# Optimization experiments

Hardware: AMD Instinct MI355X
Metric: run time of the kernel (lower is better)

Reference implementation:

```python
import jax, jax.numpy as jnp
import numpy as np

N = 8192      # nodes
E = 262144    # edges (avg degree 32)
D = 128       # embed dim
F = 128       # input feature dim
H = 128       # GCN hidden
C = 7         # classes
EPS = 1e-4    # sample_bias for concrete noise


def setup_inputs() -> dict:
    key = jax.random.key(0)
    ks = jax.random.split(key, 10)
    x = jax.random.normal(ks[0], (N, F), jnp.float32)
    embed = jax.random.normal(ks[1], (N, D), jnp.float32)
    row = jax.random.randint(ks[2], (E,), 0, N, jnp.int64)
    col = jax.random.randint(ks[3], (E,), 0, N, jnp.int64)
    adj_data = jnp.ones((E,), jnp.float32)
    # uniform noise in (bias, 1-bias) as in concrete_sample(training=True)
    noise = jax.random.uniform(ks[4], (E,), jnp.float32, EPS, 1.0 - EPS)
    tmp = jnp.ones((1,), jnp.float32)  # temperature beta
    W1e = jax.random.normal(ks[5], (3 * D, 64), jnp.float32) * 0.05
    b1e = jnp.zeros((64,), jnp.float32)
    W2e = jax.random.normal(ks[6], (64, 1), jnp.float32) * 0.05
    b2e = jnp.zeros((1,), jnp.float32)
    Wg0 = jax.random.normal(ks[7], (F, H), jnp.float32) * 0.05
    Wg1 = jax.random.normal(ks[8], (H, C), jnp.float32) * 0.05
    return {"x": x, "embed": embed, "adj_data": adj_data, "noise": noise,
            "tmp": tmp, "W1e": W1e, "b1e": b1e, "W2e": W2e, "b2e": b2e,
            "Wg0": Wg0, "Wg1": Wg1, "row": row, "col": col, "nodeid": 5}


def reference(x, embed, adj_data, noise, tmp, W1e, b1e, W2e, b2e, Wg0, Wg1,
              row, col, nodeid):
    # gather node embeddings per edge + self node embedding, concat -> [E, 3D]
    f1 = embed[row]
    f2 = embed[col]
    selfemb = jnp.broadcast_to(embed[nodeid][None, :], (f1.shape[0], D))
    f12self = jnp.concatenate([f1, f2, selfemb], axis=-1)
    # 2-layer explainer MLP -> per-edge logit
    h = jax.nn.relu(f12self @ W1e + b1e)
    log_alpha = (h @ W2e + b2e).reshape(-1)  # [E]
    # concrete-sigmoid reparameterization (training=True path, noise supplied)
    gate_inputs = (jnp.log(noise) - jnp.log1p(-noise) + log_alpha) / tmp[0]
    values = jax.nn.sigmoid(gate_inputs)
    # scatter edge gates and adjacency values into dense [N, N]
    mask = jnp.zeros((N, N), jnp.float32).at[row, col].add(values)
    adj = jnp.zeros((N, N), jnp.float32).at[row, col].add(adj_data)
    # symmetrize mask, apply to adjacency, zero the diagonal
    sym_mask = (mask + mask.T) * 0.5
    masked_adj = adj * sym_mask * (1.0 - jnp.eye(N, dtype=jnp.float32))
    # wrapped GNN: 2-layer GCN
    h1 = jax.nn.relu(masked_adj @ (x @ Wg0))
    out = masked_adj @ (h1 @ Wg1)
    node_pred = out[nodeid]  # [C]
    return jax.nn.softmax(node_pred, axis=0)
```

## Files before the change

### kernel.cpp

```cpp
#include <hip/hip_runtime.h>
#include <hip/hip_bf16.h>
#include <math.h>

#define NNODES 8192
#define DIM 128
#define SMAX 128
#define HSIZE 16384
#define NBD 256
#define NTD 1024
#define LDA 132

__device__ __forceinline__ int detect64(const void* rowp) {
    const long long* p = (const long long*)rowp;
    int is64 = 1;
#pragma unroll
    for (int i = 0; i < 4; i++) {
        long long v = p[i];
        if (v < 0 || v >= NNODES) is64 = 0;
    }
    return is64;
}

__device__ __forceinline__ int edge_idx(const void* p, int e, int idx64) {
    if (idx64) return (int)((const long long*)p)[e];
    return ((const int*)p)[e];
}

__device__ __forceinline__ int hash_insert(unsigned int* hashK, unsigned int key1) {
    unsigned int h = (key1 * 2654435761u) & (HSIZE - 1);
    for (;;) {
        unsigned int prev = atomicCAS(&hashK[h], 0u, key1);
        if (prev == 0u || prev == key1) return (int)h;
        h = (h + 1) & (HSIZE - 1);
    }
}

__global__ __launch_bounds__(256) void k_zero(float4* z, int n4) {
    int i = blockIdx.x * blockDim.x + threadIdx.x;
    if (i < n4) z[i] = make_float4(0.f, 0.f, 0.f, 0.f);
}

__global__ __launch_bounds__(NTD) void k_dense(
        const float* embed, const float* x, const float* W1e, const float* b1e,
        const float* Wg0, const int* nodep, const void* rowp, const void* colp,
        const float* adjd,
        float* U, float* V, float* xw, float* cself,
        int* flags, float* cnt0, int* nbr, int* slotmap, int E) {
    int bid = blockIdx.x;
    int t = threadIdx.x;
    int w = t >> 6;
    int lane = t & 63;
    int nodeid = nodep[0];
    __shared__ float smf[64 * LDA];
    __shared__ float semb[DIM];

    int tile = bid;
    const float* src = (tile < 128) ? embed + (size_t)tile * 64 * DIM
                                    : x + (size_t)(tile - 128) * 64 * DIM;
    for (int i = t; i < 64 * DIM; i += NTD)
        smf[(i >> 7) * LDA + (i & 127)] = src[i];
    if (bid == 255 && t < DIM) semb[t] = embed[(size_t)nodeid * DIM + t];
    __syncthreads();

    const float* Wsrc;
    float* outp;
    int ldw, ldo, cb, doff;
    if (tile < 128) {
        Wsrc = W1e; ldw = 64; ldo = 64;
        if (w < 8) { doff = 0;   cb = w * 8;       outp = U; }
        else       { doff = 128; cb = (w - 8) * 8; outp = V; }
    } else {
        Wsrc = Wg0; ldw = DIM; ldo = DIM; doff = 0; cb = w * 8; outp = xw;
    }

    int row = lane;
    float acc[8] = {0, 0, 0, 0, 0, 0, 0, 0};
    for (int d0 = 0; d0 < DIM; d0 += 8) {
        float wb = Wsrc[(size_t)(doff + d0 + (lane >> 3)) * ldw + cb + (lane & 7)];
        float4 a0 = *(const float4*)&smf[row * LDA + d0];
        float4 a1 = *(const float4*)&smf[row * LDA + d0 + 4];
#pragma unroll
        for (int k = 0; k < 8; k++) {
            float a = (k < 4) ? (&a0.x)[k] : (&a1.x)[k - 4];
#pragma unroll
            for (int j = 0; j < 8; j++) {
                float wv = __uint_as_float(
                    __builtin_amdgcn_readlane(__float_as_uint(wb), k * 8 + j));
                acc[j] = fmaf(a, wv, acc[j]);
            }
        }
    }
    int n0 = (tile < 128 ? tile : tile - 128) * 64;
    float* orow = outp + (size_t)(n0 + row) * ldo + cb;
    *(float4*)orow       = make_float4(acc[0], acc[1], acc[2], acc[3]);
    *(float4*)(orow + 4) = make_float4(acc[4], acc[5], acc[6], acc[7]);

    if (bid == 255 && t < 64) {
        float a = b1e[t];
        for (int d = 0; d < DIM; d++)
            a += semb[d] * W1e[(size_t)(2 * DIM + d) * 64 + t];
        cself[t] = a;
    }
    int idx64 = detect64(rowp);
    int e = bid * NTD + t;
    if (e < E) {
        int r = edge_idx(rowp, e, idx64);
        if (r == nodeid) {
            int c = edge_idx(colp, e, idx64);
            if (c != nodeid) {
                atomicAdd(&cnt0[c], adjd[e]);
                if (atomicCAS((unsigned int*)&slotmap[c], 0u, 0xFFFFFFFFu) == 0u) {
                    int s = atomicAdd(&flags[1], 1);
                    if (s < SMAX) {
                        nbr[s] = c;
                        __hip_atomic_store(&slotmap[c], s + 1, __ATOMIC_RELAXED,
                                           __HIP_MEMORY_SCOPE_AGENT);
                    }
                }
            }
        }
    }
}

__global__ __launch_bounds__(1024) void k_gates(
        const float* adjd, const float* noise, const float* tmp,
        const float* W2e, const float* b2e,
        const void* rowp, const void* colp, const int* nodep,
        const float* U, const float* V, const float* cself,
        const int* slotmap,
        unsigned int* hashK, float* hashC, float* hashF, float* hashR,
        float* f0s, float* r0s, int E) {
    int idx64 = detect64(rowp);
    int nodeid = nodep[0];
    int e = blockIdx.x * blockDim.x + threadIdx.x;
    if (e >= E) return;
    int r = edge_idx(rowp, e, idx64);
    int c = edge_idx(colp, e, idx64);
    if (r == c) return;
    int spr = slotmap[r];
    int spc = slotmap[c];
    bool fr = spr > 0, fc = spc > 0;
    if (!fr && !fc) return;
    float la = b2e[0];
    const float4* u4 = (const float4*)(U + (size_t)r * 64);
    const float4* v4 = (const float4*)(V + (size_t)c * 64);
    const float4* c4 = (const float4*)cself;
    const float4* w4 = (const float4*)W2e;
#pragma unroll
    for (int d = 0; d < 16; d++) {
        float4 uu = u4[d], vv = v4[d], cc = c4[d], ww = w4[d];
        float h0 = uu.x + vv.x + cc.x;
        float h1 = uu.y + vv.y + cc.y;
        float h2 = uu.z + vv.z + cc.z;
        float h3 = uu.w + vv.w + cc.w;
        la += (h0 > 0.f ? h0 : 0.f) * ww.x + (h1 > 0.f ? h1 : 0.f) * ww.y
            + (h2 > 0.f ? h2 : 0.f) * ww.z + (h3 > 0.f ? h3 : 0.f) * ww.w;
    }
    float nz = noise[e];
    float gi = (logf(nz) - log1pf(-nz) + la) / tmp[0];
    float v = 1.f / (1.f + expf(-gi));
    if (fr) {
        int sr = spr - 1;
        unsigned int key1 = ((unsigned int)(sr << 13) | (unsigned int)c) + 1u;
        int idx = hash_insert(hashK, key1);
        atomicAdd(&hashC[idx], adjd[e]);
        atomicAdd(&hashF[idx], v);
        if (c == nodeid) atomicAdd(&r0s[sr], v);
    }
    if (fc) {
        int sc = spc - 1;
        unsigned int key1 = ((unsigned int)(sc << 13) | (unsigned int)r) + 1u;
        int idx = hash_insert(hashK, key1);
        atomicAdd(&hashR[idx], v);
        if (r == nodeid) atomicAdd(&f0s[sc], v);
    }
}

__global__ __launch_bounds__(1024) void k_hagg(
        const unsigned int* hashK, const float* hashC, const float* hashF,
        const float* hashR, const float* xw, float* h1acc) {
    int gid = blockIdx.x * blockDim.x + threadIdx.x;
    int group = gid >> 7;
    int tg = gid & 127;
    int ngroups = (256 * 1024) >> 7;
    for (int entry = group; entry < HSIZE; entry += ngroups) {
        unsigned int key1 = hashK[entry];
        if (key1 == 0u) continue;
        float wgt = hashC[entry] * (hashF[entry] + hashR[entry]) * 0.5f;
        if (wgt == 0.f) continue;
        unsigned int key = key1 - 1u;
        int s = (int)(key >> 13);
        int k = (int)(key & 8191u);
        atomicAdd(&h1acc[(size_t)s * DIM + tg], wgt * xw[(size_t)k * DIM + tg]);
    }
}

__global__ __launch_bounds__(1024) void k_final(
        const int* flags, const float* h1acc, const float* cnt0, const int* nbr,
        const float* f0s, const float* r0s, const float* Wg1, float* out) {
    int t = threadIdx.x;
    __shared__ float sacc[7];
    if (t < 7) sacc[t] = 0.f;
    __syncthreads();
    int ns = flags[1]; if (ns > SMAX) ns = SMAX;
    int wave = t >> 6, lane = t & 63;
    for (int s = wave; s < ns; s += 16) {
        float a0 = cnt0[nbr[s]] * (f0s[s] + r0s[s]) * 0.5f;
        float v0 = h1acc[(size_t)s * DIM + lane];
        float v1 = h1acc[(size_t)s * DIM + lane + 64];
        v0 = v0 > 0.f ? v0 : 0.f;
        v1 = v1 > 0.f ? v1 : 0.f;
        float part[7];
        for (int c = 0; c < 7; c++) {
            float p = v0 * Wg1[lane * 7 + c] + v1 * Wg1[(lane + 64) * 7 + c];
            for (int o = 32; o >= 1; o >>= 1) p += __shfl_xor(p, o, 64);
            part[c] = p;
        }
        if (lane == 0)
            for (int c = 0; c < 7; c++) atomicAdd(&sacc[c], a0 * part[c]);
    }
    __syncthreads();
    if (t == 0) {
        float v[7], m = -1e30f, ssum = 0.f;
        for (int c = 0; c < 7; c++) { v[c] = sacc[c]; if (v[c] > m) m = v[c]; }
        for (int c = 0; c < 7; c++) { v[c] = expf(v[c] - m); ssum += v[c]; }
        for (int c = 0; c < 7; c++) out[c] = v[c] / ssum;
    }
}

extern "C" void kernel_launch(void* const* d_in, const int* in_sizes, int n_in,
                              void* d_out, int out_size, void* d_ws, size_t ws_size,
                              hipStream_t stream) {
    const float* x     = (const float*)d_in[0];
    const float* embed = (const float*)d_in[1];
    const float* adjd  = (const float*)d_in[2];
    const float* noise = (const float*)d_in[3];
    const float* tmp   = (const float*)d_in[4];
    const float* W1e   = (const float*)d_in[5];
    const float* b1e   = (const float*)d_in[6];
    const float* W2e   = (const float*)d_in[7];
    const float* b2e   = (const float*)d_in[8];
    const float* Wg0   = (const float*)d_in[9];
    const float* Wg1   = (const float*)d_in[10];
    const void*  rowp  = d_in[11];
    const void*  colp  = d_in[12];
    const int*   nodep = (const int*)d_in[13];
    int E = in_sizes[3];

    char* w = (char*)d_ws;
    size_t off = 0;
    auto alloc = [&](size_t bytes) -> char* {
        char* p = w + off;
        off = (off + bytes + 255) & ~(size_t)255;
        return p;
    };
    float*        cself   = (float*)alloc(64 * 4);
    int*          nbr     = (int*)  alloc(SMAX * 4);
    float*        U       = (float*)alloc((size_t)NNODES * 64 * 4);
    float*        V       = (float*)alloc((size_t)NNODES * 64 * 4);
    float*        xw      = (float*)alloc((size_t)NNODES * DIM * 4);
    char*         zstart  = w + off;
    int*          flags   = (int*)  alloc(256);
    int*          slotmap = (int*)  alloc((size_t)NNODES * 4);
    float*        cnt0    = (float*)alloc((size_t)NNODES * 4);
    float*        f0s     = (float*)alloc(SMAX * 4);
    float*        r0s     = (float*)alloc(SMAX * 4);
    unsigned int* hashK   = (unsigned int*)alloc((size_t)HSIZE * 4);
    float*        hashC   = (float*)alloc((size_t)HSIZE * 4);
    float*        hashF   = (float*)alloc((size_t)HSIZE * 4);
    float*        hashR   = (float*)alloc((size_t)HSIZE * 4);
    float*        h1acc   = (float*)alloc((size_t)SMAX * DIM * 4);
    size_t zbytes  = (size_t)((w + off) - zstart);
    int n4 = (int)(zbytes / 16);

    k_zero<<<(n4 + 255) / 256, 256, 0, stream>>>((float4*)zstart, n4);
    k_dense<<<NBD, NTD, 0, stream>>>(embed, x, W1e, b1e, Wg0, nodep, rowp, colp,
                                     adjd, U, V, xw, cself, flags, cnt0, nbr,
                                     slotmap, E);
    k_gates<<<E / 1024, 1024, 0, stream>>>(adjd, noise, tmp, W2e, b2e,
                                           rowp, colp, nodep, U, V, cself,
                                           slotmap, hashK, hashC, hashF, hashR,
                                           f0s, r0s, E);
    k_hagg<<<256, 1024, 0, stream>>>(hashK, hashC, hashF, hashR, xw, h1acc);
    k_final<<<1, 1024, 0, stream>>>(flags, h1acc, cnt0, nbr, f0s, r0s, Wg1,
                                    (float*)d_out);
}
```

Before: 53.38 us.

## Retile dense GEMM with LDS weights and fuse aggregation with final softmax

```diff
diff --git a/kernel.cpp b/kernel.cpp
--- a/kernel.cpp
+++ b/kernel.cpp
@@ -6,9 +6,10 @@
 #define DIM 128
 #define SMAX 128
 #define HSIZE 16384
-#define NBD 256
-#define NTD 1024
-#define LDA 132
+#define LDAT 132
+#define LDW 68
+#define NSF 128
+#define LCAP 512
 
 __device__ __forceinline__ int detect64(const void* rowp) {
     const long long* p = (const long long*)rowp;
@@ -40,7 +41,7 @@
     if (i < n4) z[i] = make_float4(0.f, 0.f, 0.f, 0.f);
 }
 
-__global__ __launch_bounds__(NTD) void k_dense(
+__global__ __launch_bounds__(512) void k_dense(
         const float* embed, const float* x, const float* W1e, const float* b1e,
         const float* Wg0, const int* nodep, const void* rowp, const void* colp,
         const float* adjd,
@@ -48,75 +49,85 @@
         int* flags, float* cnt0, int* nbr, int* slotmap, int E) {
     int bid = blockIdx.x;
     int t = threadIdx.x;
-    int w = t >> 6;
-    int lane = t & 63;
     int nodeid = nodep[0];
-    __shared__ float smf[64 * LDA];
+    int tile = bid >> 1;
+    int colh = bid & 1;
+
+    __shared__ float At[128 * LDAT];
+    __shared__ float Wl[128 * LDW];
     __shared__ float semb[DIM];
 
-    int tile = bid;
-    const float* src = (tile < 128) ? embed + (size_t)tile * 64 * DIM
-                                    : x + (size_t)(tile - 128) * 64 * DIM;
-    for (int i = t; i < 64 * DIM; i += NTD)
-        smf[(i >> 7) * LDA + (i & 127)] = src[i];
-    if (bid == 255 && t < DIM) semb[t] = embed[(size_t)nodeid * DIM + t];
+    const float* Asrc = (tile < 64) ? embed + (size_t)tile * 128 * DIM
+                                    : x + (size_t)(tile - 64) * 128 * DIM;
+    for (int i = t; i < 128 * DIM; i += 512)
+        At[(i & 127) * LDAT + (i >> 7)] = Asrc[i];
+    if (tile < 64) {
+        int doff = colh * 128;
+        for (int i = t; i < 128 * 64; i += 512)
+            Wl[(i >> 6) * LDW + (i & 63)] = W1e[(size_t)(doff + (i >> 6)) * 64 + (i & 63)];
+    } else {
+        for (int i = t; i < 128 * 64; i += 512)
+            Wl[(i >> 6) * LDW + (i & 63)] = Wg0[(size_t)(i >> 6) * DIM + colh * 64 + (i & 63)];
+    }
+    if (bid == 0 && t < DIM) semb[t] = embed[(size_t)nodeid * DIM + t];
     __syncthreads();
 
-    const float* Wsrc;
-    float* outp;
-    int ldw, ldo, cb, doff;
-    if (tile < 128) {
-        Wsrc = W1e; ldw = 64; ldo = 64;
-        if (w < 8) { doff = 0;   cb = w * 8;       outp = U; }
-        else       { doff = 128; cb = (w - 8) * 8; outp = V; }
+    int rg = t & 31;
+    int cg = t >> 5;
+    float acc[4][4];
+#pragma unroll
+    for (int i = 0; i < 4; i++)
+#pragma unroll
+        for (int j = 0; j < 4; j++) acc[i][j] = 0.f;
+
+#pragma unroll 4
+    for (int d = 0; d < DIM; d++) {
+        float4 a4 = *(const float4*)&At[d * LDAT + rg * 4];
+        float4 w4 = *(const float4*)&Wl[d * LDW + cg * 4];
+        const float* ap = &a4.x;
+        const float* wp = &w4.x;
+#pragma unroll
+        for (int i = 0; i < 4; i++)
+#pragma unroll
+            for (int j = 0; j < 4; j++)
+                acc[i][j] = fmaf(ap[i], wp[j], acc[i][j]);
+    }
+
+    if (tile < 64) {
+        float* o = colh ? V : U;
+        int n0 = tile * 128;
+#pragma unroll
+        for (int i = 0; i < 4; i++)
+            *(float4*)&o[(size_t)(n0 + rg * 4 + i) * 64 + cg * 4] =
+                make_float4(acc[i][0], acc[i][1], acc[i][2], acc[i][3]);
     } else {
-        Wsrc = Wg0; ldw = DIM; ldo = DIM; doff = 0; cb = w * 8; outp = xw;
-    }
-
-    int row = lane;
-    float acc[8] = {0, 0, 0, 0, 0, 0, 0, 0};
-    for (int d0 = 0; d0 < DIM; d0 += 8) {
-        float wb = Wsrc[(size_t)(doff + d0 + (lane >> 3)) * ldw + cb + (lane & 7)];
-        float4 a0 = *(const float4*)&smf[row * LDA + d0];
-        float4 a1 = *(const float4*)&smf[row * LDA + d0 + 4];
-#pragma unroll
-        for (int k = 0; k < 8; k++) {
-            float a = (k < 4) ? (&a0.x)[k] : (&a1.x)[k - 4];
-#pragma unroll
-            for (int j = 0; j < 8; j++) {
-                float wv = __uint_as_float(
-                    __builtin_amdgcn_readlane(__float_as_uint(wb), k * 8 + j));
-                acc[j] = fmaf(a, wv, acc[j]);
-            }
-        }
-    }
-    int n0 = (tile < 128 ? tile : tile - 128) * 64;
-    float* orow = outp + (size_t)(n0 + row) * ldo + cb;
-    *(float4*)orow       = make_float4(acc[0], acc[1], acc[2], acc[3]);
-    *(float4*)(orow + 4) = make_float4(acc[4], acc[5], acc[6], acc[7]);
-
-    if (bid == 255 && t < 64) {
+        int n0 = (tile - 64) * 128;
+#pragma unroll
+        for (int i = 0; i < 4; i++)
+            *(float4*)&xw[(size_t)(n0 + rg * 4 + i) * DIM + colh * 64 + cg * 4] =
+                make_float4(acc[i][0], acc[i][1], acc[i][2], acc[i][3]);
+    }
+
+    if (bid == 0 && t < 64) {
         float a = b1e[t];
         for (int d = 0; d < DIM; d++)
             a += semb[d] * W1e[(size_t)(2 * DIM + d) * 64 + t];
         cself[t] = a;
     }
+
     int idx64 = detect64(rowp);
-    int e = bid * NTD + t;
-    if (e < E) {
+    for (int e = bid * 512 + t; e < E; e += 256 * 512) {
         int r = edge_idx(rowp, e, idx64);
-        if (r == nodeid) {
-            int c = edge_idx(colp, e, idx64);
-            if (c != nodeid) {
-                atomicAdd(&cnt0[c], adjd[e]);
-                if (atomicCAS((unsigned int*)&slotmap[c], 0u, 0xFFFFFFFFu) == 0u) {
-                    int s = atomicAdd(&flags[1], 1);
-                    if (s < SMAX) {
-                        nbr[s] = c;
-                        __hip_atomic_store(&slotmap[c], s + 1, __ATOMIC_RELAXED,
-                                           __HIP_MEMORY_SCOPE_AGENT);
-                    }
-                }
+        if (r != nodeid) continue;
+        int c = edge_idx(colp, e, idx64);
+        if (c == nodeid) continue;
+        atomicAdd(&cnt0[c], adjd[e]);
+        if (atomicCAS((unsigned int*)&slotmap[c], 0u, 0xFFFFFFFFu) == 0u) {
+            int s = atomicAdd(&flags[1], 1);
+            if (s < SMAX) {
+                nbr[s] = c;
+                __hip_atomic_store(&slotmap[c], s + 1, __ATOMIC_RELAXED,
+                                   __HIP_MEMORY_SCOPE_AGENT);
             }
         }
     }
@@ -176,55 +187,71 @@
     }
 }
 
-__global__ __launch_bounds__(1024) void k_hagg(
-        const unsigned int* hashK, const float* hashC, const float* hashF,
-        const float* hashR, const float* xw, float* h1acc) {
-    int gid = blockIdx.x * blockDim.x + threadIdx.x;
-    int group = gid >> 7;
-    int tg = gid & 127;
-    int ngroups = (256 * 1024) >> 7;
-    for (int entry = group; entry < HSIZE; entry += ngroups) {
-        unsigned int key1 = hashK[entry];
-        if (key1 == 0u) continue;
-        float wgt = hashC[entry] * (hashF[entry] + hashR[entry]) * 0.5f;
-        if (wgt == 0.f) continue;
-        unsigned int key = key1 - 1u;
-        int s = (int)(key >> 13);
-        int k = (int)(key & 8191u);
-        atomicAdd(&h1acc[(size_t)s * DIM + tg], wgt * xw[(size_t)k * DIM + tg]);
-    }
-}
-
-__global__ __launch_bounds__(1024) void k_final(
-        const int* flags, const float* h1acc, const float* cnt0, const int* nbr,
-        const float* f0s, const float* r0s, const float* Wg1, float* out) {
-    int t = threadIdx.x;
-    __shared__ float sacc[7];
-    if (t < 7) sacc[t] = 0.f;
-    __syncthreads();
+__global__ __launch_bounds__(256) void k_slotfinal(
+        const int* flags, const unsigned int* hashK, const float* hashC,
+        const float* hashF, const float* hashR, const float* xw,
+        const float* cnt0, const int* nbr, const float* f0s, const float* r0s,
+        const float* Wg1, float* glogits, int* done, float* out) {
+    int b = blockIdx.x, t = threadIdx.x;
     int ns = flags[1]; if (ns > SMAX) ns = SMAX;
-    int wave = t >> 6, lane = t & 63;
-    for (int s = wave; s < ns; s += 16) {
-        float a0 = cnt0[nbr[s]] * (f0s[s] + r0s[s]) * 0.5f;
-        float v0 = h1acc[(size_t)s * DIM + lane];
-        float v1 = h1acc[(size_t)s * DIM + lane + 64];
-        v0 = v0 > 0.f ? v0 : 0.f;
-        v1 = v1 > 0.f ? v1 : 0.f;
-        float part[7];
-        for (int c = 0; c < 7; c++) {
-            float p = v0 * Wg1[lane * 7 + c] + v1 * Wg1[(lane + 64) * 7 + c];
-            for (int o = 32; o >= 1; o >>= 1) p += __shfl_xor(p, o, 64);
-            part[c] = p;
-        }
-        if (lane == 0)
-            for (int c = 0; c < 7; c++) atomicAdd(&sacc[c], a0 * part[c]);
+    if (b < ns) {
+        __shared__ float h1s[2][DIM];
+        __shared__ int lk[LCAP];
+        __shared__ float lw[LCAP];
+        __shared__ int lcnt;
+        __shared__ float sacc[7];
+        if (t == 0) lcnt = 0;
+        if (t < 7) sacc[t] = 0.f;
+        __syncthreads();
+        for (int e = t; e < HSIZE; e += 256) {
+            unsigned int key1 = hashK[e];
+            if (key1 == 0u) continue;
+            unsigned int key = key1 - 1u;
+            if ((int)(key >> 13) != b) continue;
+            float wgt = hashC[e] * (hashF[e] + hashR[e]) * 0.5f;
+            if (wgt == 0.f) continue;
+            int pos = atomicAdd(&lcnt, 1);
+            if (pos < LCAP) { lk[pos] = (int)(key & 8191u); lw[pos] = wgt; }
+        }
+        __syncthreads();
+        int cnt = lcnt; if (cnt > LCAP) cnt = LCAP;
+        int d = t & 127, half = t >> 7;
+        float acc = 0.f;
+        for (int i = half; i < cnt; i += 2)
+            acc += lw[i] * xw[(size_t)lk[i] * DIM + d];
+        h1s[half][d] = acc;
+        __syncthreads();
+        if (t < DIM) {
+            float hv = h1s[0][t] + h1s[1][t];
+            hv = hv > 0.f ? hv : 0.f;
+#pragma unroll
+            for (int c = 0; c < 7; c++)
+                atomicAdd(&sacc[c], hv * Wg1[t * 7 + c]);
+        }
+        __syncthreads();
+        if (t == 0) {
+            float a0 = cnt0[nbr[b]] * (f0s[b] + r0s[b]) * 0.5f;
+#pragma unroll
+            for (int c = 0; c < 7; c++)
+                atomicAdd(&glogits[c], a0 * sacc[c]);
+        }
     }
     __syncthreads();
     if (t == 0) {
-        float v[7], m = -1e30f, ssum = 0.f;
-        for (int c = 0; c < 7; c++) { v[c] = sacc[c]; if (v[c] > m) m = v[c]; }
-        for (int c = 0; c < 7; c++) { v[c] = expf(v[c] - m); ssum += v[c]; }
-        for (int c = 0; c < 7; c++) out[c] = v[c] / ssum;
+        __threadfence();
+        int old = __hip_atomic_fetch_add(done, 1, __ATOMIC_ACQ_REL,
+                                         __HIP_MEMORY_SCOPE_AGENT);
+        if (old == NSF - 1) {
+            __builtin_amdgcn_fence(__ATOMIC_ACQUIRE, "agent");
+            float v[7], m = -1e30f, ssum = 0.f;
+            for (int c = 0; c < 7; c++) {
+                v[c] = __hip_atomic_load(&glogits[c], __ATOMIC_RELAXED,
+                                         __HIP_MEMORY_SCOPE_AGENT);
+                if (v[c] > m) m = v[c];
+            }
+            for (int c = 0; c < 7; c++) { v[c] = expf(v[c] - m); ssum += v[c]; }
+            for (int c = 0; c < 7; c++) out[c] = v[c] / ssum;
+        }
     }
 }
 
@@ -261,6 +288,7 @@
     float*        xw      = (float*)alloc((size_t)NNODES * DIM * 4);
     char*         zstart  = w + off;
     int*          flags   = (int*)  alloc(256);
+    float*        glogits = (float*)alloc(256);
     int*          slotmap = (int*)  alloc((size_t)NNODES * 4);
     float*        cnt0    = (float*)alloc((size_t)NNODES * 4);
     float*        f0s     = (float*)alloc(SMAX * 4);
@@ -269,19 +297,18 @@
     float*        hashC   = (float*)alloc((size_t)HSIZE * 4);
     float*        hashF   = (float*)alloc((size_t)HSIZE * 4);
     float*        hashR   = (float*)alloc((size_t)HSIZE * 4);
-    float*        h1acc   = (float*)alloc((size_t)SMAX * DIM * 4);
     size_t zbytes  = (size_t)((w + off) - zstart);
     int n4 = (int)(zbytes / 16);
 
     k_zero<<<(n4 + 255) / 256, 256, 0, stream>>>((float4*)zstart, n4);
-    k_dense<<<NBD, NTD, 0, stream>>>(embed, x, W1e, b1e, Wg0, nodep, rowp, colp,
+    k_dense<<<256, 512, 0, stream>>>(embed, x, W1e, b1e, Wg0, nodep, rowp, colp,
                                      adjd, U, V, xw, cself, flags, cnt0, nbr,
                                      slotmap, E);
     k_gates<<<E / 1024, 1024, 0, stream>>>(adjd, noise, tmp, W2e, b2e,
                                            rowp, colp, nodep, U, V, cself,
                                            slotmap, hashK, hashC, hashF, hashR,
                                            f0s, r0s, E);
-    k_hagg<<<256, 1024, 0, stream>>>(hashK, hashC, hashF, hashR, xw, h1acc);
-    k_final<<<1, 1024, 0, stream>>>(flags, h1acc, cnt0, nbr, f0s, r0s, Wg1,
-                                    (float*)d_out);
-}
+    k_slotfinal<<<NSF, 256, 0, stream>>>(flags, hashK, hashC, hashF, hashR, xw,
+                                         cnt0, nbr, f0s, r0s, Wg1, glogits,
+                                         &flags[2], (float*)d_out);
+}
```

Measured after the change: 83.15 us. 55.8% more time.
